# Kernel tuning notes

Hardware: AMD Instinct MI355X
Metric: run time of the kernel (lower is better)

## Reference

```python
import jax, jax.numpy as jnp
import numpy as np

B, N, M, H, NH = 128, 4096, 64, 512, 4
IN, OUT = 256, 256
NH2 = 2 * NH  # read/write heads interleaved: even idx = read, odd idx = write
EPS = 1e-8


def setup_inputs() -> dict:
    key = jax.random.key(0)
    ks = jax.random.split(key, 20)
    nrm = lambda k, shape, s=0.05: (jax.random.normal(k, shape, jnp.float32) * s)
    return {
        'in_data': jax.random.normal(ks[0], (B, IN), jnp.float32),
        'memory': jax.random.normal(ks[1], (B, N, M), jnp.float32) * 0.1,
        'h_prev': jax.random.normal(ks[2], (B, H), jnp.float32),
        'c_prev': jax.random.normal(ks[3], (B, H), jnp.float32),
        'prev_reads': jax.random.normal(ks[4], (NH, B, M), jnp.float32),
        'prev_weights': jax.random.uniform(ks[5], (NH2, B, N), jnp.float32),
        # controller LSTMCell (input = in_data ++ prev_reads)
        'W_ih': nrm(ks[6], (4 * H, IN + NH * M)),
        'b_ih': jnp.zeros((4 * H,), jnp.float32),
        'W_hh': nrm(ks[7], (4 * H, H)),
        'b_hh': jnp.zeros((4 * H,), jnp.float32),
        # output layer over [h ++ reads]
        'W_out': nrm(ks[8], (OUT, H + NH * M)),
        'b_out': jnp.zeros((OUT,), jnp.float32),
        # per-head addressing params, stacked over the 2*NH heads (fed with c-state)
        'Wk': nrm(ks[9], (NH2, M, H)), 'bk': jnp.zeros((NH2, M), jnp.float32),
        'Wbeta': nrm(ks[10], (NH2, H)), 'bbeta': jnp.zeros((NH2,), jnp.float32),
        'Wg': nrm(ks[11], (NH2, H)), 'bg': jnp.zeros((NH2,), jnp.float32),
        'Ws': nrm(ks[12], (NH2, 3, H)), 'bs': jnp.zeros((NH2, 3), jnp.float32),
        'Wgam': nrm(ks[13], (NH2, H)), 'bgam': jnp.zeros((NH2,), jnp.float32),
        'We': nrm(ks[14], (NH2, M, H)), 'be': jnp.zeros((NH2, M), jnp.float32),
        'Wa': nrm(ks[15], (NH2, M, H)), 'ba': jnp.zeros((NH2, M), jnp.float32),
    }


def reference(in_data, memory, h_prev, c_prev, prev_reads, prev_weights,
              W_ih, b_ih, W_hh, b_hh, W_out, b_out,
              Wk, bk, Wbeta, bbeta, Wg, bg, Ws, bs, Wgam, bgam, We, be, Wa, ba):
    bsz = in_data.shape[0]
    # controller LSTM step on [x ++ prev_reads]
    x = jnp.concatenate([in_data, jnp.swapaxes(prev_reads, 0, 1).reshape(bsz, -1)], axis=-1)
    gates = x @ W_ih.T + h_prev @ W_hh.T + b_ih + b_hh
    gi, gf, gg, go = jnp.split(gates, 4, axis=-1)
    c = jax.nn.sigmoid(gf) * c_prev + jax.nn.sigmoid(gi) * jnp.tanh(gg)
    h = jax.nn.sigmoid(go) * jnp.tanh(c)  # |h| < 1, so clamp(-20, 20) is identity

    mem = memory
    reads = []
    for i in range(NH2):  # fixed small loop; even = read head, odd = write head
        keyv = c @ Wk[i].T + bk[i]                                    # [B, M]
        beta = jax.nn.softplus(c @ Wbeta[i] + bbeta[i])[:, None]      # [B, 1]
        g = jax.nn.sigmoid(c @ Wg[i] + bg[i])[:, None]                # [B, 1]
        s = jax.nn.softmax(c @ Ws[i].T + bs[i], axis=-1)              # [B, 3]
        gamma = 1.0 + jax.nn.softplus(c @ Wgam[i] + bgam[i])[:, None]  # [B, 1]
        # content addressing: cosine similarity, sharpened softmax
        sim = jnp.einsum('bnm,bm->bn', mem, keyv)
        sim = sim / (jnp.linalg.norm(mem, axis=-1) * jnp.linalg.norm(keyv, axis=-1, keepdims=True) + EPS)
        wc = jax.nn.softmax(beta * sim, axis=-1)
        # interpolate, circular shift (-1, 0, +1), sharpen
        wg_ = g * wc + (1.0 - g) * prev_weights[i]
        wsft = (s[:, 0:1] * jnp.roll(wg_, -1, axis=1)
                + s[:, 1:2] * wg_
                + s[:, 2:3] * jnp.roll(wg_, 1, axis=1))
        wpow = wsft ** gamma
        w = wpow / (jnp.sum(wpow, axis=1, keepdims=True) + EPS)
        if i % 2 == 0:
            reads.append(jnp.einsum('bn,bnm->bm', w, mem))
        else:
            e = jax.nn.sigmoid(c @ We[i].T + be[i])                   # erase [B, M]
            a = jnp.tanh(c @ Wa[i].T + ba[i])                         # add   [B, M]
            mem = mem * (1.0 - w[:, :, None] * e[:, None, :]) + w[:, :, None] * a[:, None, :]

    out = jax.nn.sigmoid(jnp.concatenate([h] + reads, axis=-1) @ W_out.T + b_out)
    return out
```

## Files before the change

### kernel.cpp

```cpp
#include <hip/hip_runtime.h>
#include <math.h>

#define BSZ 128
#define NN_ 4096
#define MM_ 64
#define HH_ 512
#define EPSF 1e-8f

__device__ __forceinline__ float sigmoidf_(float x) { return 1.0f / (1.0f + expf(-x)); }
__device__ __forceinline__ float softplusf_(float x) { return fmaxf(x, 0.0f) + log1pf(expf(-fabsf(x))); }

__global__ __launch_bounds__(256) void k_gemm_gates(const float* __restrict__ in_data,
                                                    const float* __restrict__ prev_reads,
                                                    const float* __restrict__ h_prev,
                                                    const float* __restrict__ W_ih,
                                                    const float* __restrict__ W_hh,
                                                    float* __restrict__ C) {
    __shared__ float Alds[64 * 129];
    __shared__ float Wlds[64 * 65];
    int t = threadIdx.x;
    int k0 = blockIdx.y * 64;
    int n0 = blockIdx.x * 64;
    for (int i = 0; i < 8; ++i) {
        int f = t + 256 * i;
        int row = f >> 4, kk = (f & 15) * 4;
        int k = k0 + kk;
        float4 v;
        if (k < 256) v = *(const float4*)(in_data + (row << 8) + k);
        else if (k < 512) {
            int q = k - 256;
            v = *(const float4*)(prev_reads + (((q >> 6) * BSZ + row) << 6) + (q & 63));
        } else v = *(const float4*)(h_prev + (row << 9) + (k - 512));
        Alds[(kk + 0) * 129 + row] = v.x;
        Alds[(kk + 1) * 129 + row] = v.y;
        Alds[(kk + 2) * 129 + row] = v.z;
        Alds[(kk + 3) * 129 + row] = v.w;
    }
    for (int i = 0; i < 4; ++i) {
        int f = t + 256 * i;
        int o = f >> 4, kk = (f & 15) * 4;
        int j = n0 + o, k = k0 + kk;
        const float* src = (k < 512) ? (W_ih + (size_t)j * 512 + k)
                                     : (W_hh + (size_t)j * 512 + (k - 512));
        float4 v = *(const float4*)src;
        Wlds[(kk + 0) * 65 + o] = v.x;
        Wlds[(kk + 1) * 65 + o] = v.y;
        Wlds[(kk + 2) * 65 + o] = v.z;
        Wlds[(kk + 3) * 65 + o] = v.w;
    }
    __syncthreads();
    int ob = (t & 15) * 4;
    int bb = (t >> 4) * 8;
    float acc[4][8];
#pragma unroll
    for (int i = 0; i < 4; ++i)
#pragma unroll
        for (int j = 0; j < 8; ++j) acc[i][j] = 0.f;
    for (int kk = 0; kk < 64; ++kk) {
        const float* wp = &Wlds[kk * 65 + ob];
        const float* ap = &Alds[kk * 129 + bb];
        float w0 = wp[0], w1 = wp[1], w2 = wp[2], w3 = wp[3];
#pragma unroll
        for (int j = 0; j < 8; ++j) {
            float av = ap[j];
            acc[0][j] = fmaf(w0, av, acc[0][j]);
            acc[1][j] = fmaf(w1, av, acc[1][j]);
            acc[2][j] = fmaf(w2, av, acc[2][j]);
            acc[3][j] = fmaf(w3, av, acc[3][j]);
        }
    }
#pragma unroll
    for (int i = 0; i < 4; ++i)
#pragma unroll
        for (int j = 0; j < 8; ++j)
            atomicAdd(&C[(size_t)(bb + j) * 2048 + n0 + ob + i], acc[i][j]);
}

__device__ __forceinline__ const float* whead_row_ptr(const float* Wk, const float* Wbeta,
                                                      const float* Wg, const float* Ws,
                                                      const float* Wgam, const float* We,
                                                      const float* Wa, int r) {
    int i = r / 198, q = r - i * 198;
    if (q < 64)  return Wk + (size_t)((i << 6) + q) * 512;
    if (q == 64) return Wbeta + (size_t)i * 512;
    if (q == 65) return Wg + (size_t)i * 512;
    if (q <= 68) return Ws + (size_t)(i * 3 + q - 66) * 512;
    if (q == 69) return Wgam + (size_t)i * 512;
    if (q < 134) return We + (size_t)((i << 6) + q - 70) * 512;
    return Wa + (size_t)((i << 6) + q - 134) * 512;
}

__global__ __launch_bounds__(256) void k_gemm_head(const float* __restrict__ A,
                                                   const float* __restrict__ Wk,
                                                   const float* __restrict__ Wbeta,
                                                   const float* __restrict__ Wg,
                                                   const float* __restrict__ Ws,
                                                   const float* __restrict__ Wgam,
                                                   const float* __restrict__ We,
                                                   const float* __restrict__ Wa,
                                                   float* __restrict__ C) {
    __shared__ float Alds[64 * 129];
    __shared__ float Wlds[64 * 65];
    int t = threadIdx.x;
    int k0 = blockIdx.y * 64;
    int n0 = blockIdx.x * 64;
    for (int i = 0; i < 8; ++i) {
        int f = t + 256 * i;
        int row = f >> 4, kk = (f & 15) * 4;
        float4 v = *(const float4*)(A + (size_t)row * 512 + k0 + kk);
        Alds[(kk + 0) * 129 + row] = v.x;
        Alds[(kk + 1) * 129 + row] = v.y;
        Alds[(kk + 2) * 129 + row] = v.z;
        Alds[(kk + 3) * 129 + row] = v.w;
    }
    for (int i = 0; i < 4; ++i) {
        int f = t + 256 * i;
        int o = f >> 4, kk = (f & 15) * 4;
        int r = n0 + o;
        float4 v = make_float4(0.f, 0.f, 0.f, 0.f);
        if (r < 1386) {
            const float* p = whead_row_ptr(Wk, Wbeta, Wg, Ws, Wgam, We, Wa, r) + k0 + kk;
            v = *(const float4*)p;
        }
        Wlds[(kk + 0) * 65 + o] = v.x;
        Wlds[(kk + 1) * 65 + o] = v.y;
        Wlds[(kk + 2) * 65 + o] = v.z;
        Wlds[(kk + 3) * 65 + o] = v.w;
    }
    __syncthreads();
    int ob = (t & 15) * 4;
    int bb = (t >> 4) * 8;
    float acc[4][8];
#pragma unroll
    for (int i = 0; i < 4; ++i)
#pragma unroll
        for (int j = 0; j < 8; ++j) acc[i][j] = 0.f;
    for (int kk = 0; kk < 64; ++kk) {
        const float* wp = &Wlds[kk * 65 + ob];
        const float* ap = &Alds[kk * 129 + bb];
        float w0 = wp[0], w1 = wp[1], w2 = wp[2], w3 = wp[3];
#pragma unroll
        for (int j = 0; j < 8; ++j) {
            float av = ap[j];
            acc[0][j] = fmaf(w0, av, acc[0][j]);
            acc[1][j] = fmaf(w1, av, acc[1][j]);
            acc[2][j] = fmaf(w2, av, acc[2][j]);
            acc[3][j] = fmaf(w3, av, acc[3][j]);
        }
    }
#pragma unroll
    for (int i = 0; i < 4; ++i)
#pragma unroll
        for (int j = 0; j < 8; ++j)
            atomicAdd(&C[(size_t)(bb + j) * 1408 + n0 + ob + i], acc[i][j]);
}

__global__ __launch_bounds__(256) void k_gemm_out(const float* __restrict__ hbuf,
                                                  const float* __restrict__ rbuf,
                                                  const float* __restrict__ W_out,
                                                  float* __restrict__ C) {
    __shared__ float Alds[64 * 129];
    __shared__ float Wlds[64 * 65];
    int t = threadIdx.x;
    int k0 = blockIdx.y * 64;
    int n0 = blockIdx.x * 64;
    for (int i = 0; i < 8; ++i) {
        int f = t + 256 * i;
        int row = f >> 4, kk = (f & 15) * 4;
        int k = k0 + kk;
        float4 v;
        if (k < 512) v = *(const float4*)(hbuf + (row << 9) + k);
        else {
            int q = k - 512;
            v = *(const float4*)(rbuf + (((q >> 6) * BSZ + row) << 6) + (q & 63));
        }
        Alds[(kk + 0) * 129 + row] = v.x;
        Alds[(kk + 1) * 129 + row] = v.y;
        Alds[(kk + 2) * 129 + row] = v.z;
        Alds[(kk + 3) * 129 + row] = v.w;
    }
    for (int i = 0; i < 4; ++i) {
        int f = t + 256 * i;
        int o = f >> 4, kk = (f & 15) * 4;
        float4 v = *(const float4*)(W_out + (size_t)(n0 + o) * 768 + k0 + kk);
        Wlds[(kk + 0) * 65 + o] = v.x;
        Wlds[(kk + 1) * 65 + o] = v.y;
        Wlds[(kk + 2) * 65 + o] = v.z;
        Wlds[(kk + 3) * 65 + o] = v.w;
    }
    __syncthreads();
    int ob = (t & 15) * 4;
    int bb = (t >> 4) * 8;
    float acc[4][8];
#pragma unroll
    for (int i = 0; i < 4; ++i)
#pragma unroll
        for (int j = 0; j < 8; ++j) acc[i][j] = 0.f;
    for (int kk = 0; kk < 64; ++kk) {
        const float* wp = &Wlds[kk * 65 + ob];
        const float* ap = &Alds[kk * 129 + bb];
        float w0 = wp[0], w1 = wp[1], w2 = wp[2], w3 = wp[3];
#pragma unroll
        for (int j = 0; j < 8; ++j) {
            float av = ap[j];
            acc[0][j] = fmaf(w0, av, acc[0][j]);
            acc[1][j] = fmaf(w1, av, acc[1][j]);
            acc[2][j] = fmaf(w2, av, acc[2][j]);
            acc[3][j] = fmaf(w3, av, acc[3][j]);
        }
    }
#pragma unroll
    for (int i = 0; i < 4; ++i)
#pragma unroll
        for (int j = 0; j < 8; ++j)
            atomicAdd(&C[(size_t)(bb + j) * 256 + n0 + ob + i], acc[i][j]);
}

__global__ void k_lstm(const float* __restrict__ gates, const float* __restrict__ b_ih,
                       const float* __restrict__ b_hh, const float* __restrict__ c_prev,
                       float* __restrict__ cbuf, float* __restrict__ hbuf) {
    int idx = blockIdx.x * blockDim.x + threadIdx.x;
    if (idx >= BSZ * HH_) return;
    int b = idx >> 9, j = idx & 511;
    const float* gr = gates + (size_t)b * 2048;
    float gi = gr[j]        + b_ih[j]        + b_hh[j];
    float gf = gr[512 + j]  + b_ih[512 + j]  + b_hh[512 + j];
    float gg = gr[1024 + j] + b_ih[1024 + j] + b_hh[1024 + j];
    float go = gr[1536 + j] + b_ih[1536 + j] + b_hh[1536 + j];
    float cc = sigmoidf_(gf) * c_prev[idx] + sigmoidf_(gi) * tanhf(gg);
    float hh = sigmoidf_(go) * tanhf(cc);
    cbuf[idx] = cc;
    hbuf[idx] = hh;
}

__global__ __launch_bounds__(256) void k_headact(const float* __restrict__ Chead,
                                                 const float* __restrict__ bk, const float* __restrict__ bbeta,
                                                 const float* __restrict__ bg, const float* __restrict__ bs,
                                                 const float* __restrict__ bgam, const float* __restrict__ be,
                                                 const float* __restrict__ ba,
                                                 float* __restrict__ keys, float* __restrict__ knorm,
                                                 float* __restrict__ betaA, float* __restrict__ gA,
                                                 float* __restrict__ gammaA, float* __restrict__ sA,
                                                 float* __restrict__ eA, float* __restrict__ aA) {
    __shared__ float sk[64];
    __shared__ float s3[3];
    int blk = blockIdx.x;
    int i = blk >> 7, b = blk & 127;
    int q = threadIdx.x;
    float val = 0.f;
    if (q < 198) {
        float bv = (q < 64)   ? bk[(i << 6) + q]
                 : (q == 64)  ? bbeta[i]
                 : (q == 65)  ? bg[i]
                 : (q <= 68)  ? bs[i * 3 + q - 66]
                 : (q == 69)  ? bgam[i]
                 : (q < 134)  ? be[(i << 6) + q - 70]
                              : ba[(i << 6) + q - 134];
        val = Chead[(size_t)b * 1408 + i * 198 + q] + bv;
    }
    if (q < 64) { keys[(size_t)(i * BSZ + b) * 64 + q] = val; sk[q] = val * val; }
    if (q >= 66 && q <= 68) s3[q - 66] = val;
    __syncthreads();
    if (q == 0) {
        float s = 0.f;
        for (int m2 = 0; m2 < 64; ++m2) s += sk[m2];
        knorm[i * BSZ + b] = sqrtf(s);
    }
    if (q == 64) betaA[i * BSZ + b] = softplusf_(val);
    if (q == 65) gA[i * BSZ + b] = sigmoidf_(val);
    if (q == 69) gammaA[i * BSZ + b] = 1.f + softplusf_(val);
    if (q == 66) {
        float mx = fmaxf(s3[0], fmaxf(s3[1], s3[2]));
        float e0 = expf(s3[0] - mx), e1 = expf(s3[1] - mx), e2 = expf(s3[2] - mx);
        float inv = 1.f / (e0 + e1 + e2);
        sA[(i * BSZ + b) * 3 + 0] = e0 * inv;
        sA[(i * BSZ + b) * 3 + 1] = e1 * inv;
        sA[(i * BSZ + b) * 3 + 2] = e2 * inv;
    }
    if (q >= 70 && q < 134)  eA[(size_t)(i * BSZ + b) * 64 + (q - 70)] = sigmoidf_(val);
    if (q >= 134 && q < 198) aA[(size_t)(i * BSZ + b) * 64 + (q - 134)] = tanhf(val);
}

__global__ __launch_bounds__(256) void k_pass2(const float* __restrict__ mem,
                                               const float* __restrict__ wbuf,
                                               const float* __restrict__ eA, const float* __restrict__ aA,
                                               const float* __restrict__ keys, const float* __restrict__ knorm,
                                               float* __restrict__ sims, float* __restrict__ r_out,
                                               int napply, int nsims, int sh0, int sh1,
                                               int read_state, int read_head, int read_idx) {
    __shared__ __align__(16) float rbuf[16][64];
    int t = threadIdx.x;
    int lane = t & 15, grp = t >> 4;
    int base = blockIdx.x * 64;
    int b = base >> 12;
    int m4 = lane * 4;
    float4 e1 = *(const float4*)(eA + (size_t)(1 * BSZ + b) * 64 + m4);
    float4 a1 = *(const float4*)(aA + (size_t)(1 * BSZ + b) * 64 + m4);
    float4 e3 = *(const float4*)(eA + (size_t)(3 * BSZ + b) * 64 + m4);
    float4 a3 = *(const float4*)(aA + (size_t)(3 * BSZ + b) * 64 + m4);
    float4 e5 = *(const float4*)(eA + (size_t)(5 * BSZ + b) * 64 + m4);
    float4 a5 = *(const float4*)(aA + (size_t)(5 * BSZ + b) * 64 + m4);
    float4 k0v = make_float4(0.f, 0.f, 0.f, 0.f), k1v = k0v;
    float kn0v = 0.f, kn1v = 0.f;
    if (nsims > 0) { k0v = *(const float4*)(keys + (size_t)(sh0 * BSZ + b) * 64 + m4); kn0v = knorm[sh0 * BSZ + b]; }
    if (nsims > 1) { k1v = *(const float4*)(keys + (size_t)(sh1 * BSZ + b) * 64 + m4); kn1v = knorm[sh1 * BSZ + b]; }
    const float* w1p = wbuf + (size_t)1 * BSZ * NN_;
    const float* w3p = wbuf + (size_t)3 * BSZ * NN_;
    const float* w5p = wbuf + (size_t)5 * BSZ * NN_;
    const float* wrp = (read_head >= 0) ? (wbuf + (size_t)read_head * BSZ * NN_) : nullptr;
    float* sim0 = sims + (size_t)sh0 * BSZ * NN_;
    float* sim1 = sims + (size_t)sh1 * BSZ * NN_;

    float4 racc = make_float4(0.f, 0.f, 0.f, 0.f);
    for (int it = 0; it < 4; ++it) {
        int row = base + it * 16 + grp;
        float4 m = *(const float4*)(mem + (size_t)row * 64 + m4);
        float4 mr = m;
        if (napply >= 1) {
            float w = w1p[row];
            m.x = m.x * (1.f - w * e1.x) + w * a1.x;
            m.y = m.y * (1.f - w * e1.y) + w * a1.y;
            m.z = m.z * (1.f - w * e1.z) + w * a1.z;
            m.w = m.w * (1.f - w * e1.w) + w * a1.w;
            if (read_state == 1) mr = m;
        }
        if (napply >= 2) {
            float w = w3p[row];
            m.x = m.x * (1.f - w * e3.x) + w * a3.x;
            m.y = m.y * (1.f - w * e3.y) + w * a3.y;
            m.z = m.z * (1.f - w * e3.z) + w * a3.z;
            m.w = m.w * (1.f - w * e3.w) + w * a3.w;
            if (read_state == 2) mr = m;
        }
        if (napply >= 3) {
            float w = w5p[row];
            m.x = m.x * (1.f - w * e5.x) + w * a5.x;
            m.y = m.y * (1.f - w * e5.y) + w * a5.y;
            m.z = m.z * (1.f - w * e5.z) + w * a5.z;
            m.w = m.w * (1.f - w * e5.w) + w * a5.w;
            if (read_state == 3) mr = m;
        }
        if (read_head >= 0) {
            float wr = wrp[row];
            racc.x = fmaf(wr, mr.x, racc.x);
            racc.y = fmaf(wr, mr.y, racc.y);
            racc.z = fmaf(wr, mr.z, racc.z);
            racc.w = fmaf(wr, mr.w, racc.w);
        }
        if (nsims > 0) {
            float d0 = m.x * k0v.x + m.y * k0v.y + m.z * k0v.z + m.w * k0v.w;
            float nn = m.x * m.x + m.y * m.y + m.z * m.z + m.w * m.w;
            float d1 = 0.f;
            if (nsims > 1) d1 = m.x * k1v.x + m.y * k1v.y + m.z * k1v.z + m.w * k1v.w;
#pragma unroll
            for (int off = 8; off >= 1; off >>= 1) {
                d0 += __shfl_xor(d0, off, 16);
                nn += __shfl_xor(nn, off, 16);
                if (nsims > 1) d1 += __shfl_xor(d1, off, 16);
            }
            if (lane == 0) {
                float nm = sqrtf(nn);
                sim0[row] = d0 / (nm * kn0v + EPSF);
                if (nsims > 1) sim1[row] = d1 / (nm * kn1v + EPSF);
            }
        }
    }
    if (read_head >= 0) {
        *(float4*)(&rbuf[grp][m4]) = racc;
        __syncthreads();
        if (t < 64) {
            float s = 0.f;
#pragma unroll
            for (int g2 = 0; g2 < 16; ++g2) s += rbuf[g2][t];
            atomicAdd(&r_out[(size_t)(read_idx * BSZ + b) * 64 + t], s);
        }
    }
}

__global__ __launch_bounds__(1024) void k_weights(const float* __restrict__ sims,
                                                  const float* __restrict__ prev_w,
                                                  const float* __restrict__ betaA, const float* __restrict__ gA,
                                                  const float* __restrict__ gammaA, const float* __restrict__ sA,
                                                  float* __restrict__ wout_base, int head0) {
    __shared__ float wg[NN_];
    __shared__ float redm[16], reds[16], redp[16];
    int h = head0 + blockIdx.y, b = blockIdx.x;
    int hb = h * BSZ + b;
    float beta = betaA[hb], g = gA[hb], gamma = gammaA[hb];
    float s0 = sA[hb * 3 + 0], s1 = sA[hb * 3 + 1], s2 = sA[hb * 3 + 2];
    const float* sim = sims + (size_t)hb * NN_;
    const float* pw = prev_w + (size_t)hb * NN_;
    float* wout = wout_base + (size_t)hb * NN_;
    int t = threadIdx.x, wv = t >> 6, ln = t & 63;
    float tv[4];
    float lmax = -3.4e38f;
#pragma unroll
    for (int j = 0; j < 4; ++j) {
        float x = beta * sim[t + 1024 * j];
        tv[j] = x;
        lmax = fmaxf(lmax, x);
    }
#pragma unroll
    for (int off = 32; off >= 1; off >>= 1) lmax = fmaxf(lmax, __shfl_xor(lmax, off));
    if (ln == 0) redm[wv] = lmax;
    __syncthreads();
    float Mx = redm[0];
#pragma unroll
    for (int k = 1; k < 16; ++k) Mx = fmaxf(Mx, redm[k]);
    float lsum = 0.f;
#pragma unroll
    for (int j = 0; j < 4; ++j) { float ex = expf(tv[j] - Mx); tv[j] = ex; lsum += ex; }
#pragma unroll
    for (int off = 32; off >= 1; off >>= 1) lsum += __shfl_xor(lsum, off);
    if (ln == 0) reds[wv] = lsum;
    __syncthreads();
    float S = 0.f;
#pragma unroll
    for (int k = 0; k < 16; ++k) S += reds[k];
    float invS = 1.f / S;
#pragma unroll
    for (int j = 0; j < 4; ++j) {
        int n = t + 1024 * j;
        wg[n] = g * tv[j] * invS + (1.f - g) * pw[n];
    }
    __syncthreads();
    float lsum2 = 0.f;
#pragma unroll
    for (int j = 0; j < 4; ++j) {
        int n = t + 1024 * j;
        float wsft = s0 * wg[(n + 1) & (NN_ - 1)] + s1 * wg[n] + s2 * wg[(n - 1) & (NN_ - 1)];
        float wp = powf(wsft, gamma);
        tv[j] = wp;
        lsum2 += wp;
    }
#pragma unroll
    for (int off = 32; off >= 1; off >>= 1) lsum2 += __shfl_xor(lsum2, off);
    if (ln == 0) redp[wv] = lsum2;
    __syncthreads();
    float S2 = 0.f;
#pragma unroll
    for (int k = 0; k < 16; ++k) S2 += redp[k];
    float inv2 = 1.f / (S2 + EPSF);
#pragma unroll
    for (int j = 0; j < 4; ++j) wout[t + 1024 * j] = tv[j] * inv2;
}

__global__ void k_out(const float* __restrict__ outacc, const float* __restrict__ b_out,
                      float* __restrict__ out) {
    int idx = blockIdx.x * blockDim.x + threadIdx.x;
    if (idx >= BSZ * 256) return;
    out[idx] = sigmoidf_(outacc[idx] + b_out[idx & 255]);
}

extern "C" void kernel_launch(void* const* d_in, const int* in_sizes, int n_in,
                              void* d_out, int out_size, void* d_ws, size_t ws_size,
                              hipStream_t stream) {
    const float* in_data      = (const float*)d_in[0];
    const float* memory       = (const float*)d_in[1];
    const float* h_prev       = (const float*)d_in[2];
    const float* c_prev       = (const float*)d_in[3];
    const float* prev_reads   = (const float*)d_in[4];
    const float* prev_weights = (const float*)d_in[5];
    const float* W_ih = (const float*)d_in[6];
    const float* b_ih = (const float*)d_in[7];
    const float* W_hh = (const float*)d_in[8];
    const float* b_hh = (const float*)d_in[9];
    const float* W_out = (const float*)d_in[10];
    const float* b_out = (const float*)d_in[11];
    const float* Wk   = (const float*)d_in[12];
    const float* bk   = (const float*)d_in[13];
    const float* Wbeta = (const float*)d_in[14];
    const float* bbeta = (const float*)d_in[15];
    const float* Wg   = (const float*)d_in[16];
    const float* bg   = (const float*)d_in[17];
    const float* Ws   = (const float*)d_in[18];
    const float* bs   = (const float*)d_in[19];
    const float* Wgam = (const float*)d_in[20];
    const float* bgam = (const float*)d_in[21];
    const float* We   = (const float*)d_in[22];
    const float* be   = (const float*)d_in[23];
    const float* Wa   = (const float*)d_in[24];
    const float* ba   = (const float*)d_in[25];

    float* ws = (float*)d_ws;
    size_t o_gates  = 0;
    size_t o_chead  = o_gates + 262144;
    size_t o_r      = o_chead + 180224;
    size_t o_outacc = o_r + 32768;
    size_t zero_floats = o_outacc + 32768;
    size_t o_c     = zero_floats;
    size_t o_h     = o_c + 65536;
    size_t o_keys  = o_h + 65536;
    size_t o_knorm = o_keys + 57344;
    size_t o_beta  = o_knorm + 1024;
    size_t o_g     = o_beta + 1024;
    size_t o_gamma = o_g + 1024;
    size_t o_s     = o_gamma + 1024;
    size_t o_e     = o_s + 3072;
    size_t o_a     = o_e + 57344;
    size_t o_sims  = o_a + 57344;
    size_t o_w     = o_sims + 3670016;

    float* gates  = ws + o_gates;
    float* Chead  = ws + o_chead;
    float* rbuf   = ws + o_r;
    float* outacc = ws + o_outacc;
    float* cbuf   = ws + o_c;
    float* hbuf   = ws + o_h;
    float* keys   = ws + o_keys;
    float* knorm  = ws + o_knorm;
    float* betaA  = ws + o_beta;
    float* gA     = ws + o_g;
    float* gammaA = ws + o_gamma;
    float* sA     = ws + o_s;
    float* eA     = ws + o_e;
    float* aA     = ws + o_a;
    float* sims   = ws + o_sims;
    float* wbuf   = ws + o_w;

    hipMemsetAsync(d_ws, 0, zero_floats * sizeof(float), stream);

    k_gemm_gates<<<dim3(32, 16), 256, 0, stream>>>(in_data, prev_reads, h_prev, W_ih, W_hh, gates);
    k_lstm<<<256, 256, 0, stream>>>(gates, b_ih, b_hh, c_prev, cbuf, hbuf);

    k_gemm_head<<<dim3(22, 8), 256, 0, stream>>>(cbuf, Wk, Wbeta, Wg, Ws, Wgam, We, Wa, Chead);
    k_headact<<<896, 256, 0, stream>>>(Chead, bk, bbeta, bg, bs, bgam, be, ba,
                                       keys, knorm, betaA, gA, gammaA, sA, eA, aA);

    const int PB = BSZ * NN_ / 64;
    k_pass2<<<PB, 256, 0, stream>>>(memory, wbuf, eA, aA, keys, knorm, sims, rbuf,
                                    0, 2, 0, 1, -1, -1, 0);
    k_weights<<<dim3(128, 2), 1024, 0, stream>>>(sims, prev_weights, betaA, gA, gammaA, sA, wbuf, 0);
    k_pass2<<<PB, 256, 0, stream>>>(memory, wbuf, eA, aA, keys, knorm, sims, rbuf,
                                    1, 2, 2, 3, 0, 0, 0);
    k_weights<<<dim3(128, 2), 1024, 0, stream>>>(sims, prev_weights, betaA, gA, gammaA, sA, wbuf, 2);
    k_pass2<<<PB, 256, 0, stream>>>(memory, wbuf, eA, aA, keys, knorm, sims, rbuf,
                                    2, 2, 4, 5, 1, 2, 1);
    k_weights<<<dim3(128, 2), 1024, 0, stream>>>(sims, prev_weights, betaA, gA, gammaA, sA, wbuf, 4);
    k_pass2<<<PB, 256, 0, stream>>>(memory, wbuf, eA, aA, keys, knorm, sims, rbuf,
                                    3, 1, 6, 6, 2, 4, 2);
    k_weights<<<dim3(128, 1), 1024, 0, stream>>>(sims, prev_weights, betaA, gA, gammaA, sA, wbuf, 6);
    k_pass2<<<PB, 256, 0, stream>>>(memory, wbuf, eA, aA, keys, knorm, sims, rbuf,
                                    3, 0, 0, 0, 3, 6, 3);

    k_gemm_out<<<dim3(4, 12), 256, 0, stream>>>(hbuf, rbuf, W_out, outacc);
    k_out<<<128, 256, 0, stream>>>(outacc, b_out, (float*)d_out);

    (void)in_sizes; (void)n_in; (void)out_size; (void)ws_size;
}
```

Before: 534.7 us.

## Replace atomic split-K GEMMs with partial-sum buffers and fused output GEMM

The three small GEMMs no longer accumulate through per-element atomicAdd into zeroed buffers. The gates and head GEMMs now tile over batch and write fixed split-K partials to separate slices, which the consuming LSTM and head-activation kernels sum. The output GEMM runs the full K loop in one kernel and applies bias and sigmoid directly, dropping the k_out launch. This shrinks the memset and removes atomic contention, but it uses fewer blocks, which lowers parallelism, especially for the 8-block output GEMM.

```diff
diff --git a/kernel.cpp b/kernel.cpp
--- a/kernel.cpp
+++ b/kernel.cpp
@@ -15,65 +15,94 @@
                                                     const float* __restrict__ h_prev,
                                                     const float* __restrict__ W_ih,
                                                     const float* __restrict__ W_hh,
-                                                    float* __restrict__ C) {
-    __shared__ float Alds[64 * 129];
+                                                    float* __restrict__ Cp) {
+    __shared__ float Alds[64 * 65];
     __shared__ float Wlds[64 * 65];
     int t = threadIdx.x;
-    int k0 = blockIdx.y * 64;
     int n0 = blockIdx.x * 64;
-    for (int i = 0; i < 8; ++i) {
-        int f = t + 256 * i;
-        int row = f >> 4, kk = (f & 15) * 4;
-        int k = k0 + kk;
-        float4 v;
-        if (k < 256) v = *(const float4*)(in_data + (row << 8) + k);
-        else if (k < 512) {
-            int q = k - 256;
-            v = *(const float4*)(prev_reads + (((q >> 6) * BSZ + row) << 6) + (q & 63));
-        } else v = *(const float4*)(h_prev + (row << 9) + (k - 512));
-        Alds[(kk + 0) * 129 + row] = v.x;
-        Alds[(kk + 1) * 129 + row] = v.y;
-        Alds[(kk + 2) * 129 + row] = v.z;
-        Alds[(kk + 3) * 129 + row] = v.w;
-    }
-    for (int i = 0; i < 4; ++i) {
-        int f = t + 256 * i;
-        int o = f >> 4, kk = (f & 15) * 4;
-        int j = n0 + o, k = k0 + kk;
-        const float* src = (k < 512) ? (W_ih + (size_t)j * 512 + k)
-                                     : (W_hh + (size_t)j * 512 + (k - 512));
-        float4 v = *(const float4*)src;
-        Wlds[(kk + 0) * 65 + o] = v.x;
-        Wlds[(kk + 1) * 65 + o] = v.y;
-        Wlds[(kk + 2) * 65 + o] = v.z;
-        Wlds[(kk + 3) * 65 + o] = v.w;
-    }
-    __syncthreads();
+    int b0 = blockIdx.y * 64;
+    float* C = Cp + (size_t)blockIdx.z * (BSZ * 2048);
     int ob = (t & 15) * 4;
-    int bb = (t >> 4) * 8;
-    float acc[4][8];
+    int bb = (t >> 4) * 4;
+    float acc[4][4];
 #pragma unroll
     for (int i = 0; i < 4; ++i)
 #pragma unroll
-        for (int j = 0; j < 8; ++j) acc[i][j] = 0.f;
-    for (int kk = 0; kk < 64; ++kk) {
-        const float* wp = &Wlds[kk * 65 + ob];
-        const float* ap = &Alds[kk * 129 + bb];
-        float w0 = wp[0], w1 = wp[1], w2 = wp[2], w3 = wp[3];
-#pragma unroll
-        for (int j = 0; j < 8; ++j) {
-            float av = ap[j];
-            acc[0][j] = fmaf(w0, av, acc[0][j]);
-            acc[1][j] = fmaf(w1, av, acc[1][j]);
-            acc[2][j] = fmaf(w2, av, acc[2][j]);
-            acc[3][j] = fmaf(w3, av, acc[3][j]);
+        for (int j = 0; j < 4; ++j) acc[i][j] = 0.f;
+    for (int kt = 0; kt < 4; ++kt) {
+        int k0 = blockIdx.z * 256 + kt * 64;
+        __syncthreads();
+        for (int i = 0; i < 4; ++i) {
+            int f = t + 256 * i;
+            int row = f >> 4, kk = (f & 15) * 4;
+            int k = k0 + kk;
+            float4 v;
+            if (k < 256) v = *(const float4*)(in_data + ((b0 + row) << 8) + k);
+            else if (k < 512) {
+                int q = k - 256;
+                v = *(const float4*)(prev_reads + (((q >> 6) * BSZ + b0 + row) << 6) + (q & 63));
+            } else v = *(const float4*)(h_prev + ((b0 + row) << 9) + (k - 512));
+            Alds[(kk + 0) * 65 + row] = v.x;
+            Alds[(kk + 1) * 65 + row] = v.y;
+            Alds[(kk + 2) * 65 + row] = v.z;
+            Alds[(kk + 3) * 65 + row] = v.w;
+        }
+        for (int i = 0; i < 4; ++i) {
+            int f = t + 256 * i;
+            int o = f >> 4, kk = (f & 15) * 4;
+            int j = n0 + o, k = k0 + kk;
+            const float* src = (k < 512) ? (W_ih + (size_t)j * 512 + k)
+                                         : (W_hh + (size_t)j * 512 + (k - 512));
+            float4 v = *(const float4*)src;
+            Wlds[(kk + 0) * 65 + o] = v.x;
+            Wlds[(kk + 1) * 65 + o] = v.y;
+            Wlds[(kk + 2) * 65 + o] = v.z;
+            Wlds[(kk + 3) * 65 + o] = v.w;
+        }
+        __syncthreads();
+        for (int kk = 0; kk < 64; ++kk) {
+            const float* wp = &Wlds[kk * 65 + ob];
+            const float* ap = &Alds[kk * 65 + bb];
+            float w0 = wp[0], w1 = wp[1], w2 = wp[2], w3 = wp[3];
+#pragma unroll
+            for (int j = 0; j < 4; ++j) {
+                float av = ap[j];
+                acc[0][j] = fmaf(w0, av, acc[0][j]);
+                acc[1][j] = fmaf(w1, av, acc[1][j]);
+                acc[2][j] = fmaf(w2, av, acc[2][j]);
+                acc[3][j] = fmaf(w3, av, acc[3][j]);
+            }
         }
     }
 #pragma unroll
     for (int i = 0; i < 4; ++i)
 #pragma unroll
-        for (int j = 0; j < 8; ++j)
-            atomicAdd(&C[(size_t)(bb + j) * 2048 + n0 + ob + i], acc[i][j]);
+        for (int j = 0; j < 4; ++j)
+            C[(size_t)(b0 + bb + j) * 2048 + n0 + ob + i] = acc[i][j];
+}
+
+__global__ void k_lstm(const float* __restrict__ gatesP, const float* __restrict__ b_ih,
+                       const float* __restrict__ b_hh, const float* __restrict__ c_prev,
+                       float* __restrict__ cbuf, float* __restrict__ hbuf) {
+    int idx = blockIdx.x * blockDim.x + threadIdx.x;
+    if (idx >= BSZ * HH_) return;
+    int b = idx >> 9, j = idx & 511;
+    float gi = b_ih[j]        + b_hh[j];
+    float gf = b_ih[512 + j]  + b_hh[512 + j];
+    float gg = b_ih[1024 + j] + b_hh[1024 + j];
+    float go = b_ih[1536 + j] + b_hh[1536 + j];
+#pragma unroll
+    for (int p = 0; p < 4; ++p) {
+        const float* gr = gatesP + (size_t)p * (BSZ * 2048) + (size_t)b * 2048;
+        gi += gr[j];
+        gf += gr[512 + j];
+        gg += gr[1024 + j];
+        go += gr[1536 + j];
+    }
+    float cc = sigmoidf_(gf) * c_prev[idx] + sigmoidf_(gi) * tanhf(gg);
+    float hh = sigmoidf_(go) * tanhf(cc);
+    cbuf[idx] = cc;
+    hbuf[idx] = hh;
 }
 
 __device__ __forceinline__ const float* whead_row_ptr(const float* Wk, const float* Wbeta,
@@ -98,142 +127,70 @@
                                                    const float* __restrict__ Wgam,
                                                    const float* __restrict__ We,
                                                    const float* __restrict__ Wa,
-                                                   float* __restrict__ C) {
-    __shared__ float Alds[64 * 129];
+                                                   float* __restrict__ Cp) {
+    __shared__ float Alds[64 * 65];
     __shared__ float Wlds[64 * 65];
     int t = threadIdx.x;
-    int k0 = blockIdx.y * 64;
     int n0 = blockIdx.x * 64;
-    for (int i = 0; i < 8; ++i) {
-        int f = t + 256 * i;
-        int row = f >> 4, kk = (f & 15) * 4;
-        float4 v = *(const float4*)(A + (size_t)row * 512 + k0 + kk);
-        Alds[(kk + 0) * 129 + row] = v.x;
-        Alds[(kk + 1) * 129 + row] = v.y;
-        Alds[(kk + 2) * 129 + row] = v.z;
-        Alds[(kk + 3) * 129 + row] = v.w;
-    }
-    for (int i = 0; i < 4; ++i) {
-        int f = t + 256 * i;
-        int o = f >> 4, kk = (f & 15) * 4;
-        int r = n0 + o;
-        float4 v = make_float4(0.f, 0.f, 0.f, 0.f);
-        if (r < 1386) {
-            const float* p = whead_row_ptr(Wk, Wbeta, Wg, Ws, Wgam, We, Wa, r) + k0 + kk;
-            v = *(const float4*)p;
-        }
-        Wlds[(kk + 0) * 65 + o] = v.x;
-        Wlds[(kk + 1) * 65 + o] = v.y;
-        Wlds[(kk + 2) * 65 + o] = v.z;
-        Wlds[(kk + 3) * 65 + o] = v.w;
-    }
-    __syncthreads();
+    int b0 = blockIdx.y * 64;
+    float* C = Cp + (size_t)blockIdx.z * (BSZ * 1408);
     int ob = (t & 15) * 4;
-    int bb = (t >> 4) * 8;
-    float acc[4][8];
+    int bb = (t >> 4) * 4;
+    float acc[4][4];
 #pragma unroll
     for (int i = 0; i < 4; ++i)
 #pragma unroll
-        for (int j = 0; j < 8; ++j) acc[i][j] = 0.f;
-    for (int kk = 0; kk < 64; ++kk) {
-        const float* wp = &Wlds[kk * 65 + ob];
-        const float* ap = &Alds[kk * 129 + bb];
-        float w0 = wp[0], w1 = wp[1], w2 = wp[2], w3 = wp[3];
-#pragma unroll
-        for (int j = 0; j < 8; ++j) {
-            float av = ap[j];
-            acc[0][j] = fmaf(w0, av, acc[0][j]);
-            acc[1][j] = fmaf(w1, av, acc[1][j]);
-            acc[2][j] = fmaf(w2, av, acc[2][j]);
-            acc[3][j] = fmaf(w3, av, acc[3][j]);
+        for (int j = 0; j < 4; ++j) acc[i][j] = 0.f;
+    for (int kt = 0; kt < 4; ++kt) {
+        int k0 = blockIdx.z * 256 + kt * 64;
+        __syncthreads();
+        for (int i = 0; i < 4; ++i) {
+            int f = t + 256 * i;
+            int row = f >> 4, kk = (f & 15) * 4;
+            float4 v = *(const float4*)(A + (size_t)(b0 + row) * 512 + k0 + kk);
+            Alds[(kk + 0) * 65 + row] = v.x;
+            Alds[(kk + 1) * 65 + row] = v.y;
+            Alds[(kk + 2) * 65 + row] = v.z;
+            Alds[(kk + 3) * 65 + row] = v.w;
+        }
+        for (int i = 0; i < 4; ++i) {
+            int f = t + 256 * i;
+            int o = f >> 4, kk = (f & 15) * 4;
+            int r = n0 + o;
+            float4 v = make_float4(0.f, 0.f, 0.f, 0.f);
+            if (r < 1386) {
+                const float* p = whead_row_ptr(Wk, Wbeta, Wg, Ws, Wgam, We, Wa, r) + k0 + kk;
+                v = *(const float4*)p;
+            }
+            Wlds[(kk + 0) * 65 + o] = v.x;
+            Wlds[(kk + 1) * 65 + o] = v.y;
+            Wlds[(kk + 2) * 65 + o] = v.z;
+            Wlds[(kk + 3) * 65 + o] = v.w;
+        }
+        __syncthreads();
+        for (int kk = 0; kk < 64; ++kk) {
+            const float* wp = &Wlds[kk * 65 + ob];
+            const float* ap = &Alds[kk * 65 + bb];
+            float w0 = wp[0], w1 = wp[1], w2 = wp[2], w3 = wp[3];
+#pragma unroll
+            for (int j = 0; j < 4; ++j) {
+                float av = ap[j];
+                acc[0][j] = fmaf(w0, av, acc[0][j]);
+                acc[1][j] = fmaf(w1, av, acc[1][j]);
+                acc[2][j] = fmaf(w2, av, acc[2][j]);
+                acc[3][j] = fmaf(w3, av, acc[3][j]);
+            }
         }
     }
 #pragma unroll
     for (int i = 0; i < 4; ++i)
 #pragma unroll
-        for (int j = 0; j < 8; ++j)
-            atomicAdd(&C[(size_t)(bb + j) * 1408 + n0 + ob + i], acc[i][j]);
-}
-
-__global__ __launch_bounds__(256) void k_gemm_out(const float* __restrict__ hbuf,
-                                                  const float* __restrict__ rbuf,
-                                                  const float* __restrict__ W_out,
-                                                  float* __restrict__ C) {
-    __shared__ float Alds[64 * 129];
-    __shared__ float Wlds[64 * 65];
-    int t = threadIdx.x;
-    int k0 = blockIdx.y * 64;
-    int n0 = blockIdx.x * 64;
-    for (int i = 0; i < 8; ++i) {
-        int f = t + 256 * i;
-        int row = f >> 4, kk = (f & 15) * 4;
-        int k = k0 + kk;
-        float4 v;
-        if (k < 512) v = *(const float4*)(hbuf + (row << 9) + k);
-        else {
-            int q = k - 512;
-            v = *(const float4*)(rbuf + (((q >> 6) * BSZ + row) << 6) + (q & 63));
-        }
-        Alds[(kk + 0) * 129 + row] = v.x;
-        Alds[(kk + 1) * 129 + row] = v.y;
-        Alds[(kk + 2) * 129 + row] = v.z;
-        Alds[(kk + 3) * 129 + row] = v.w;
-    }
-    for (int i = 0; i < 4; ++i) {
-        int f = t + 256 * i;
-        int o = f >> 4, kk = (f & 15) * 4;
-        float4 v = *(const float4*)(W_out + (size_t)(n0 + o) * 768 + k0 + kk);
-        Wlds[(kk + 0) * 65 + o] = v.x;
-        Wlds[(kk + 1) * 65 + o] = v.y;
-        Wlds[(kk + 2) * 65 + o] = v.z;
-        Wlds[(kk + 3) * 65 + o] = v.w;
-    }
-    __syncthreads();
-    int ob = (t & 15) * 4;
-    int bb = (t >> 4) * 8;
-    float acc[4][8];
-#pragma unroll
-    for (int i = 0; i < 4; ++i)
-#pragma unroll
-        for (int j = 0; j < 8; ++j) acc[i][j] = 0.f;
-    for (int kk = 0; kk < 64; ++kk) {
-        const float* wp = &Wlds[kk * 65 + ob];
-        const float* ap = &Alds[kk * 129 + bb];
-        float w0 = wp[0], w1 = wp[1], w2 = wp[2], w3 = wp[3];
-#pragma unroll
-        for (int j = 0; j < 8; ++j) {
-            float av = ap[j];
-            acc[0][j] = fmaf(w0, av, acc[0][j]);
-            acc[1][j] = fmaf(w1, av, acc[1][j]);
-            acc[2][j] = fmaf(w2, av, acc[2][j]);
-            acc[3][j] = fmaf(w3, av, acc[3][j]);
-        }
-    }
-#pragma unroll
-    for (int i = 0; i < 4; ++i)
-#pragma unroll
-        for (int j = 0; j < 8; ++j)
-            atomicAdd(&C[(size_t)(bb + j) * 256 + n0 + ob + i], acc[i][j]);
-}
-
-__global__ void k_lstm(const float* __restrict__ gates, const float* __restrict__ b_ih,
-                       const float* __restrict__ b_hh, const float* __restrict__ c_prev,
-                       float* __restrict__ cbuf, float* __restrict__ hbuf) {
-    int idx = blockIdx.x * blockDim.x + threadIdx.x;
-    if (idx >= BSZ * HH_) return;
-    int b = idx >> 9, j = idx & 511;
-    const float* gr = gates + (size_t)b * 2048;
-    float gi = gr[j]        + b_ih[j]        + b_hh[j];
-    float gf = gr[512 + j]  + b_ih[512 + j]  + b_hh[512 + j];
-    float gg = gr[1024 + j] + b_ih[1024 + j] + b_hh[1024 + j];
-    float go = gr[1536 + j] + b_ih[1536 + j] + b_hh[1536 + j];
-    float cc = sigmoidf_(gf) * c_prev[idx] + sigmoidf_(gi) * tanhf(gg);
-    float hh = sigmoidf_(go) * tanhf(cc);
-    cbuf[idx] = cc;
-    hbuf[idx] = hh;
-}
-
-__global__ __launch_bounds__(256) void k_headact(const float* __restrict__ Chead,
+        for (int j = 0; j < 4; ++j)
+            C[(size_t)(b0 + bb + j) * 1408 + n0 + ob + i] = acc[i][j];
+}
+
+__global__ __launch_bounds__(256) void k_headact(const float* __restrict__ C0,
+                                                 const float* __restrict__ C1,
                                                  const float* __restrict__ bk, const float* __restrict__ bbeta,
                                                  const float* __restrict__ bg, const float* __restrict__ bs,
                                                  const float* __restrict__ bgam, const float* __restrict__ be,
@@ -256,7 +213,8 @@
                  : (q == 69)  ? bgam[i]
                  : (q < 134)  ? be[(i << 6) + q - 70]
                               : ba[(i << 6) + q - 134];
-        val = Chead[(size_t)b * 1408 + i * 198 + q] + bv;
+        size_t idx = (size_t)b * 1408 + i * 198 + q;
+        val = C0[idx] + C1[idx] + bv;
     }
     if (q < 64) { keys[(size_t)(i * BSZ + b) * 64 + q] = val; sk[q] = val * val; }
     if (q >= 66 && q <= 68) s3[q - 66] = val;
@@ -445,11 +403,69 @@
     for (int j = 0; j < 4; ++j) wout[t + 1024 * j] = tv[j] * inv2;
 }
 
-__global__ void k_out(const float* __restrict__ outacc, const float* __restrict__ b_out,
-                      float* __restrict__ out) {
-    int idx = blockIdx.x * blockDim.x + threadIdx.x;
-    if (idx >= BSZ * 256) return;
-    out[idx] = sigmoidf_(outacc[idx] + b_out[idx & 255]);
+__global__ __launch_bounds__(256) void k_out_full(const float* __restrict__ hbuf,
+                                                  const float* __restrict__ rbuf,
+                                                  const float* __restrict__ W_out,
+                                                  const float* __restrict__ b_out,
+                                                  float* __restrict__ out) {
+    __shared__ float Alds[64 * 65];
+    __shared__ float Wlds[64 * 65];
+    int t = threadIdx.x;
+    int n0 = blockIdx.x * 64;
+    int b0 = blockIdx.y * 64;
+    int ob = (t & 15) * 4;
+    int bb = (t >> 4) * 4;
+    float acc[4][4];
+#pragma unroll
+    for (int i = 0; i < 4; ++i)
+#pragma unroll
+        for (int j = 0; j < 4; ++j) acc[i][j] = 0.f;
+    for (int k0 = 0; k0 < 768; k0 += 64) {
+        __syncthreads();
+        for (int i = 0; i < 4; ++i) {
+            int f = t + 256 * i;
+            int rb = f >> 4, kk = (f & 15) * 4;
+            int k = k0 + kk;
+            float4 v;
+            if (k < 512) v = *(const float4*)(hbuf + ((b0 + rb) << 9) + k);
+            else {
+                int q = k - 512;
+                v = *(const float4*)(rbuf + (((q >> 6) * BSZ + b0 + rb) << 6) + (q & 63));
+            }
+            Alds[(kk + 0) * 65 + rb] = v.x;
+            Alds[(kk + 1) * 65 + rb] = v.y;
+            Alds[(kk + 2) * 65 + rb] = v.z;
+            Alds[(kk + 3) * 65 + rb] = v.w;
+        }
+        for (int i = 0; i < 4; ++i) {
+            int f = t + 256 * i;
+            int o = f >> 4, kk = (f & 15) * 4;
+            float4 v = *(const float4*)(W_out + (size_t)(n0 + o) * 768 + k0 + kk);
+            Wlds[(kk + 0) * 65 + o] = v.x;
+            Wlds[(kk + 1) * 65 + o] = v.y;
+            Wlds[(kk + 2) * 65 + o] = v.z;
+            Wlds[(kk + 3) * 65 + o] = v.w;
+        }
+        __syncthreads();
+        for (int kk = 0; kk < 64; ++kk) {
+            const float* wp = &Wlds[kk * 65 + ob];
+            const float* ap = &Alds[kk * 65 + bb];
+            float w0 = wp[0], w1 = wp[1], w2 = wp[2], w3 = wp[3];
+#pragma unroll
+            for (int j = 0; j < 4; ++j) {
+                float av = ap[j];
+                acc[0][j] = fmaf(w0, av, acc[0][j]);
+                acc[1][j] = fmaf(w1, av, acc[1][j]);
+                acc[2][j] = fmaf(w2, av, acc[2][j]);
+                acc[3][j] = fmaf(w3, av, acc[3][j]);
+            }
+        }
+    }
+#pragma unroll
+    for (int i = 0; i < 4; ++i)
+#pragma unroll
+        for (int j = 0; j < 4; ++j)
+            out[(size_t)(b0 + bb + j) * 256 + n0 + ob + i] = sigmoidf_(acc[i][j] + b_out[n0 + ob + i]);
 }
 
 extern "C" void kernel_launch(void* const* d_in, const int* in_sizes, int n_in,
@@ -483,12 +499,11 @@
     const float* ba   = (const float*)d_in[25];
 
     float* ws = (float*)d_ws;
-    size_t o_gates  = 0;
-    size_t o_chead  = o_gates + 262144;
-    size_t o_r      = o_chead + 180224;
-    size_t o_outacc = o_r + 32768;
-    size_t zero_floats = o_outacc + 32768;
-    size_t o_c     = zero_floats;
+    size_t o_r      = 0;
+    size_t zero_floats = 32768;
+    size_t o_gatesP = zero_floats;
+    size_t o_cheadP = o_gatesP + 1048576;
+    size_t o_c     = o_cheadP + 360448;
     size_t o_h     = o_c + 65536;
     size_t o_keys  = o_h + 65536;
     size_t o_knorm = o_keys + 57344;
@@ -501,10 +516,9 @@
     size_t o_sims  = o_a + 57344;
     size_t o_w     = o_sims + 3670016;
 
-    float* gates  = ws + o_gates;
-    float* Chead  = ws + o_chead;
     float* rbuf   = ws + o_r;
-    float* outacc = ws + o_outacc;
+    float* gatesP = ws + o_gatesP;
+    float* CheadP = ws + o_cheadP;
     float* cbuf   = ws + o_c;
     float* hbuf   = ws + o_h;
     float* keys   = ws + o_keys;
@@ -520,11 +534,12 @@
 
     hipMemsetAsync(d_ws, 0, zero_floats * sizeof(float), stream);
 
-    k_gemm_gates<<<dim3(32, 16), 256, 0, stream>>>(in_data, prev_reads, h_prev, W_ih, W_hh, gates);
-    k_lstm<<<256, 256, 0, stream>>>(gates, b_ih, b_hh, c_prev, cbuf, hbuf);
-
-    k_gemm_head<<<dim3(22, 8), 256, 0, stream>>>(cbuf, Wk, Wbeta, Wg, Ws, Wgam, We, Wa, Chead);
-    k_headact<<<896, 256, 0, stream>>>(Chead, bk, bbeta, bg, bs, bgam, be, ba,
+    k_gemm_gates<<<dim3(32, 2, 4), 256, 0, stream>>>(in_data, prev_reads, h_prev, W_ih, W_hh, gatesP);
+    k_lstm<<<256, 256, 0, stream>>>(gatesP, b_ih, b_hh, c_prev, cbuf, hbuf);
+
+    k_gemm_head<<<dim3(22, 2, 2), 256, 0, stream>>>(cbuf, Wk, Wbeta, Wg, Ws, Wgam, We, Wa, CheadP);
+    k_headact<<<896, 256, 0, stream>>>(CheadP, CheadP + (size_t)BSZ * 1408,
+                                       bk, bbeta, bg, bs, bgam, be, ba,
                                        keys, knorm, betaA, gA, gammaA, sA, eA, aA);
 
     const int PB = BSZ * NN_ / 64;
@@ -543,8 +558,7 @@
     k_pass2<<<PB, 256, 0, stream>>>(memory, wbuf, eA, aA, keys, knorm, sims, rbuf,
                                     3, 0, 0, 0, 3, 6, 3);
 
-    k_gemm_out<<<dim3(4, 12), 256, 0, stream>>>(hbuf, rbuf, W_out, outacc);
-    k_out<<<128, 256, 0, stream>>>(outacc, b_out, (float*)d_out);
+    k_out_full<<<dim3(4, 2), 256, 0, stream>>>(hbuf, rbuf, W_out, b_out, (float*)d_out);
 
     (void)in_sizes; (void)n_in; (void)out_size; (void)ws_size;
 }
```

Result: no change. 529.8 us, median of 2 (-0.9%).
